# Kernel tuning notes

Hardware: AMD Instinct MI355X
Metric: run time of the kernel (lower is better)

Reference implementation:

```python
import jax, jax.numpy as jnp
import numpy as np

B, T, HOP = 4, 200, 120
N = T * HOP
M1, A1 = 40, 5            # mcep_order+1, apdc_order+1
HID, COND = 256, 192
SR = 24000.0
ALPHA = 0.466             # frequency-warping for 24 kHz
PD = 4                    # Pade order
PADE = jnp.asarray([1.0, 0.4999273, 0.1067005, 0.00956526, 0.0003041358], jnp.float32)
SIGN = jnp.asarray([1.0, -1.0, 1.0, -1.0], jnp.float32)  # + for odd Pade tap index
F0_MEAN, F0_STD = 5.0, 0.25
MCEP_MEAN, MCEP_STD = 0.0, 1.0
APDC_MEAN, APDC_STD = 0.0, 1.0
NOISE_RATIO, SP_RATE, F0_RATE = 0.5, 1.0, 1.0


def mc2b(mc, a):
    """SPTK mc2b: mel-cepstrum -> MLSA filter coefficients (scan over order)."""
    mc_rev = jnp.moveaxis(mc, -1, 0)[::-1]  # [M1, B, T]
    def step(carry, c):
        b = c - a * carry
        return b, b
    _, bs = jax.lax.scan(step, jnp.zeros_like(mc_rev[0]), mc_rev)
    return jnp.moveaxis(bs[::-1], 0, -1)


def _mlsafir(x, b, d):
    # SPTK mlsafir, vectorized over the PD Pade taps.
    # x: [PD], b: [M1], d: [PD, M1+1]
    aa = 1.0 - ALPHA * ALPHA
    d1 = aa * x + ALPHA * d[:, 1]
    def step(prev, di):  # d_new[i] = d[i] + a*(d[i+1] - d_new[i-1]) : order recurrence
        d_i, d_ip1 = di
        new = d_i + ALPHA * (d_ip1 - prev)
        return new, new
    xs = (d[:, 2:M1].T, d[:, 3:M1 + 1].T)  # [M1-2, PD]
    _, dupd = jax.lax.scan(step, d1, xs)    # [M1-2, PD]
    y = jnp.einsum('mp,m->p', dupd, b[2:])
    # delay-line shift: new d = [x, d1, d1, dupd[2..M]]
    new_d = jnp.concatenate([x[:, None], d1[:, None], d1[:, None], dupd.T], axis=1)
    return y, new_d


def _mlsa_step(state, inp):
    d1a, d1b, d2, pt2 = state
    x, b = inp
    x = x * jnp.exp(b[0])           # gain
    # ---- stage 1 (uses b[1] only), SPTK mlsadf1 ----
    aa = 1.0 - ALPHA * ALPHA
    na = aa * d1b[:PD] + ALPHA * d1a[1:]
    npt = na * b[1]
    v1 = npt * PADE[1:]
    x1 = x + jnp.sum(v1 * SIGN)
    y1 = jnp.sum(v1) + x1
    d1a = jnp.concatenate([d1a[:1], na])
    d1b = jnp.concatenate([x1[None], npt])
    # ---- stage 2 (orders >= 2), SPTK mlsadf2 ----
    fy, d2 = _mlsafir(pt2[:PD], b, d2)
    v2 = fy * PADE[1:]
    x2 = y1 + jnp.sum(v2 * SIGN)
    y2 = jnp.sum(v2) + x2
    pt2 = jnp.concatenate([x2[None], fy])
    return (d1a, d1b, d2, pt2), y2


def mlsa_filter(exc, b_up):
    # exc: [N], b_up: [N, M1] -> filtered waveform [N]
    init = (jnp.zeros(PD + 1, jnp.float32), jnp.zeros(PD + 1, jnp.float32),
            jnp.zeros((PD, M1 + 1), jnp.float32), jnp.zeros(PD + 1, jnp.float32))
    _, y = jax.lax.scan(_mlsa_step, init, (exc, b_up))
    return y


def _forward(mceps, apdcs, frame_f0s, noise,
             Wm, bm, Wa, ba, Wf, bf, Wpa, bpa, Wpp, bpp,
             Wrp, brp, Wra, bra, Wap):
    # linear feature embed + sum
    hs = mceps @ Wm + bm + apdcs @ Wa + ba + frame_f0s @ Wf + bf   # [B,T,HID]
    ca = hs @ Wpa + bpa                                             # prenet_a cond [B,T,COND]
    cp = hs @ Wpp + bpp                                             # prenet_p cond
    # denorm (+ exp for log-f0)
    f0 = jnp.exp(frame_f0s[..., 0] * F0_STD + F0_MEAN) * F0_RATE    # [B,T]
    sp = mceps * MCEP_STD + MCEP_MEAN
    ap = apdcs * APDC_STD + APDC_MEAN
    # per-path mel-cepstra with prenet residuals
    mc_p = sp * SP_RATE + 0.1 * jnp.tanh(cp @ Wrp + brp)
    mc_a = sp * SP_RATE + 0.1 * jnp.tanh(ca @ Wra + bra) + ap @ Wap
    b_p = mc2b(mc_p, ALPHA)
    b_a = mc2b(mc_a, ALPHA)
    # excitation at sample rate
    f0_up = jnp.repeat(f0, HOP, axis=1)                             # [B,N]
    phase = jnp.cumsum(f0_up / SR, axis=1)
    w = jnp.floor(phase)
    wprev = jnp.concatenate([jnp.zeros_like(w[:, :1]), w[:, :-1]], axis=1)
    amp = jnp.sqrt(SR / jnp.maximum(f0_up, 1.0))
    pulse = jnp.where(w > wprev, amp, 0.0)
    exc_p = pulse * (1.0 - NOISE_RATIO)
    exc_a = noise * NOISE_RATIO
    # run both (periodic/aperiodic) MLSA synthesis filters in one batched scan
    excs = jnp.concatenate([exc_p, exc_a], axis=0)                  # [2B,N]
    bs = jnp.repeat(jnp.concatenate([b_p, b_a], axis=0), HOP, axis=1)  # [2B,N,M1]
    wavs = jax.vmap(mlsa_filter)(excs, bs)                          # [2B,N]
    return wavs[:B] + wavs[B:]


_forward_jit = jax.jit(_forward)


def setup_inputs() -> dict:
    key = jax.random.key(0)
    ks = jax.random.split(key, 20)
    decay = 0.3 / (1.0 + jnp.arange(M1, dtype=jnp.float32))  # realistic cepstral decay (filter stability)
    return {
        'mceps': jax.random.normal(ks[0], (B, T, M1), jnp.float32) * decay,
        'apdcs': jax.random.normal(ks[1], (B, T, A1), jnp.float32) * 0.3,
        'frame_f0s': jax.random.normal(ks[2], (B, T, 1), jnp.float32),
        'noise': jax.random.normal(ks[3], (B, N), jnp.float32),
        'Wm': jax.random.normal(ks[4], (M1, HID), jnp.float32) / np.sqrt(M1),
        'bm': jnp.zeros((HID,), jnp.float32),
        'Wa': jax.random.normal(ks[5], (A1, HID), jnp.float32) / np.sqrt(A1),
        'ba': jnp.zeros((HID,), jnp.float32),
        'Wf': jax.random.normal(ks[6], (1, HID), jnp.float32),
        'bf': jnp.zeros((HID,), jnp.float32),
        'Wpa': jax.random.normal(ks[7], (HID, COND), jnp.float32) / np.sqrt(HID),
        'bpa': jnp.zeros((COND,), jnp.float32),
        'Wpp': jax.random.normal(ks[8], (HID, COND), jnp.float32) / np.sqrt(HID),
        'bpp': jnp.zeros((COND,), jnp.float32),
        'Wrp': jax.random.normal(ks[9], (COND, M1), jnp.float32) / np.sqrt(COND),
        'brp': jnp.zeros((M1,), jnp.float32),
        'Wra': jax.random.normal(ks[10], (COND, M1), jnp.float32) / np.sqrt(COND),
        'bra': jnp.zeros((M1,), jnp.float32),
        'Wap': jax.random.normal(ks[11], (A1, M1), jnp.float32) * 0.05,
    }


def reference(mceps, apdcs, frame_f0s, noise,
              Wm, bm, Wa, ba, Wf, bf, Wpa, bpa, Wpp, bpp,
              Wrp, brp, Wra, bra, Wap):
    return _forward_jit(mceps, apdcs, frame_f0s, noise,
                        Wm, bm, Wa, ba, Wf, bf, Wpa, bpa, Wpp, bpp,
                        Wrp, brp, Wra, bra, Wap)
```

## Files before the change

### kernel.cpp

```cpp
#include <hip/hip_runtime.h>
#include <math.h>

#define ALPHA 0.466f
#define T_FRAMES 200
#define HOPW 120
#define NSAMP 24000
#define M1 40
#define HID 256
#define CONDW 192

#define NCHUNK 200
#define WARMF 4
#define SERF (WARMF + 1)
#define WARMK0 96

#define F8 8
#define EMB_BLOCKS (4 * T_FRAMES / F8)
#define BPF ((NSAMP + 255) / 256)

#if defined(__has_builtin)
#  if __has_builtin(__builtin_amdgcn_permlane32_swap)
#    define HAVE_PLSWAP 1
#  endif
#endif
#ifndef HAVE_PLSWAP
#  define HAVE_PLSWAP 0
#endif

__global__ __launch_bounds__(256) void prep_kernel(
    const float* __restrict__ mceps, const float* __restrict__ apdcs,
    const float* __restrict__ f0s, const float* __restrict__ noise,
    const float* __restrict__ Wm, const float* __restrict__ bm,
    const float* __restrict__ Wa, const float* __restrict__ ba,
    const float* __restrict__ Wf, const float* __restrict__ bf,
    const float* __restrict__ Wpa, const float* __restrict__ bpa,
    const float* __restrict__ Wpp, const float* __restrict__ bpp,
    const float* __restrict__ Wrp, const float* __restrict__ brp,
    const float* __restrict__ Wra, const float* __restrict__ bra,
    const float* __restrict__ Wap,
    float* __restrict__ bcoef, float* __restrict__ exc)
{
    const int tid = threadIdx.x;

    if (blockIdx.x >= EMB_BLOCKS) {
        const int xb = blockIdx.x - EMB_BLOCKS;
        const int ff = xb / BPF;
        const int n = (xb % BPF) * 256 + tid;

        if (ff >= 4) {
            if (n < NSAMP) exc[ff * NSAMP + n] = 0.5f * noise[(ff - 4) * NSAMP + n];
            return;
        }

        __shared__ double s_base[T_FRAMES];
        __shared__ double s_step[T_FRAMES];
        __shared__ float  s_amp[T_FRAMES];

        if (tid < 64) {
            const int L = tid;
            double st[4], loc[4];
            float am[4];
            double s = 0.0;
            #pragma unroll
            for (int j = 0; j < 4; ++j) {
                int ft = L * 4 + j;
                if (ft < T_FRAMES) {
                    double fv = exp((double)f0s[ff * T_FRAMES + ft] * 0.25 + 5.0);
                    st[j] = fv / 24000.0;
                    am[j] = (float)(0.5 * sqrt(24000.0 / fmax(fv, 1.0)));
                } else { st[j] = 0.0; am[j] = 0.f; }
                loc[j] = s;
                s += st[j];
            }
            double tot = s;
            #pragma unroll
            for (int off = 1; off < 64; off <<= 1) {
                double v = __shfl_up(s, off, 64);
                if (L >= off) s += v;
            }
            double excl = s - tot;
            #pragma unroll
            for (int j = 0; j < 4; ++j) {
                int ft = L * 4 + j;
                if (ft < T_FRAMES) {
                    s_base[ft] = 120.0 * (excl + loc[j]);
                    s_step[ft] = st[j];
                    s_amp[ft]  = am[j];
                }
            }
        }
        __syncthreads();

        if (n < NSAMP) {
            int ft = n / HOPW, k = n - ft * HOPW;
            double st = s_step[ft], bs = s_base[ft];
            double ph  = bs + (double)(k + 1) * st;
            double php = bs + (double)k * st;
            exc[ff * NSAMP + n] = (floor(ph) > floor(php)) ? s_amp[ft] : 0.0f;
        }
        return;
    }

    __shared__ float s_mc[F8][M1];
    __shared__ float s_ap[F8][5];
    __shared__ float s_f0[F8];
    __shared__ float s_h[F8][HID];
    __shared__ float s_ca[F8][CONDW];
    __shared__ float s_cp[F8][CONDW];
    __shared__ float s_mcp[F8][M1];
    __shared__ float s_mca[F8][M1];

    const int R0 = blockIdx.x * F8;

    for (int j = tid; j < F8 * M1; j += 256) s_mc[j / M1][j % M1] = mceps[R0 * M1 + j];
    if (tid < F8 * 5) s_ap[tid / 5][tid % 5] = apdcs[R0 * 5 + tid];
    if (tid < F8)     s_f0[tid] = f0s[R0 + tid];
    __syncthreads();

    {
        float acc[F8];
        const float bias = bm[tid] + ba[tid] + bf[tid];
        #pragma unroll
        for (int r = 0; r < F8; ++r) acc[r] = bias;
        for (int k = 0; k < M1; ++k) {
            float w = Wm[k * HID + tid];
            #pragma unroll
            for (int r = 0; r < F8; ++r) acc[r] = fmaf(s_mc[r][k], w, acc[r]);
        }
        #pragma unroll
        for (int k = 0; k < 5; ++k) {
            float w = Wa[k * HID + tid];
            #pragma unroll
            for (int r = 0; r < F8; ++r) acc[r] = fmaf(s_ap[r][k], w, acc[r]);
        }
        float wf = Wf[tid];
        #pragma unroll
        for (int r = 0; r < F8; ++r) s_h[r][tid] = fmaf(s_f0[r], wf, acc[r]);
    }
    __syncthreads();

    if (tid < CONDW) {
        float aA[F8], aP[F8];
        #pragma unroll
        for (int r = 0; r < F8; ++r) { aA[r] = bpa[tid]; aP[r] = bpp[tid]; }
        for (int k = 0; k < HID; k += 4) {
            float4 h4[F8];
            #pragma unroll
            for (int r = 0; r < F8; ++r) h4[r] = *(const float4*)&s_h[r][k];
            #pragma unroll
            for (int kk = 0; kk < 4; ++kk) {
                float wa = Wpa[(k + kk) * CONDW + tid];
                float wp = Wpp[(k + kk) * CONDW + tid];
                #pragma unroll
                for (int r = 0; r < F8; ++r) {
                    float hv = (&h4[r].x)[kk];
                    aA[r] = fmaf(hv, wa, aA[r]);
                    aP[r] = fmaf(hv, wp, aP[r]);
                }
            }
        }
        #pragma unroll
        for (int r = 0; r < F8; ++r) { s_ca[r][tid] = aA[r]; s_cp[r][tid] = aP[r]; }
    }
    __syncthreads();

    if (tid < M1) {
        const int u = tid;
        float acc[F8];
        #pragma unroll
        for (int r = 0; r < F8; ++r) acc[r] = brp[u];
        for (int k = 0; k < CONDW; k += 4) {
            float4 c4[F8];
            #pragma unroll
            for (int r = 0; r < F8; ++r) c4[r] = *(const float4*)&s_cp[r][k];
            #pragma unroll
            for (int kk = 0; kk < 4; ++kk) {
                float w = Wrp[(k + kk) * M1 + u];
                #pragma unroll
                for (int r = 0; r < F8; ++r) acc[r] = fmaf((&c4[r].x)[kk], w, acc[r]);
            }
        }
        #pragma unroll
        for (int r = 0; r < F8; ++r)
            s_mcp[r][u] = s_mc[r][u] + 0.1f * tanhf(acc[r]);
    } else if (tid >= 64 && tid < 64 + M1) {
        const int u = tid - 64;
        float acc[F8];
        #pragma unroll
        for (int r = 0; r < F8; ++r) acc[r] = bra[u];
        for (int k = 0; k < CONDW; k += 4) {
            float4 c4[F8];
            #pragma unroll
            for (int r = 0; r < F8; ++r) c4[r] = *(const float4*)&s_ca[r][k];
            #pragma unroll
            for (int kk = 0; kk < 4; ++kk) {
                float w = Wra[(k + kk) * M1 + u];
                #pragma unroll
                for (int r = 0; r < F8; ++r) acc[r] = fmaf((&c4[r].x)[kk], w, acc[r]);
            }
        }
        #pragma unroll
        for (int r = 0; r < F8; ++r) {
            float aw = 0.f;
            #pragma unroll
            for (int j = 0; j < 5; ++j) aw = fmaf(s_ap[r][j], Wap[j * M1 + u], aw);
            s_mca[r][u] = s_mc[r][u] + 0.1f * tanhf(acc[r]) + aw;
        }
    }
    __syncthreads();

    if (tid < 16) {
        const int r = tid >> 1, path = tid & 1;
        const int R = R0 + r;
        const int batch = R / T_FRAMES, t = R - batch * T_FRAMES;
        const float* src = path ? s_mca[r] : s_mcp[r];
        float* dst = bcoef + ((path * 4 + batch) * T_FRAMES + t) * M1;
        float prev = src[M1 - 1];
        dst[M1 - 1] = prev;
        for (int m = M1 - 2; m >= 0; --m) {
            prev = src[m] - ALPHA * prev;
            dst[m] = prev;
        }
    }
}

template <int CTRL>
__device__ __forceinline__ float rshr(float x) {
    return __int_as_float(
        __builtin_amdgcn_mov_dpp(__float_as_int(x), CTRL, 0xF, 0xF, true));
}
__device__ __forceinline__ float rlane(float x, int l) {
    return __int_as_float(__builtin_amdgcn_readlane(__float_as_int(x), l));
}
__device__ __forceinline__ float vpin(float x) {
    asm("" : "+v"(x));
    return x;
}

template <bool OUT, int KSTART>
__device__ __forceinline__ void run_frame(
    const float* __restrict__ sx, float AB,
    float BP1, float BP2, float BP3, float BP4,
    float B0, float B1, float B2, float B3, float B4,
    float K, float IPw, bool pos0, bool row0, bool parodd,
    float& E0, float& E1, float& E2, float& E3, float& E4,
    float& dlp, float& xin,
    float& m1, float& m2, float& m3, float& m4, float& w0,
    float* __restrict__ yb)
{
    const float A   = ALPHA;
    const float AA  = 1.0f - A * A;
    const float A2  = A * A;
    const float mA3 = -(A * A2);
    const float A4  = A2 * A2;
    const float R   = -(A4 * A);
    const float R2  = R * R;

    const float Rv   = vpin(R);
    const float R2v  = vpin(R2);
    const float IPwv = vpin(IPw);

    #pragma unroll 1
    for (int k8 = KSTART; k8 < HOPW; k8 += 8) {
        const float4 g0 = *(const float4*)&sx[k8];
        const float4 g1 = *(const float4*)&sx[k8 + 4];
        const float xs[8] = {g0.x, g0.y, g0.z, g0.w, g1.x, g1.y, g1.z, g1.w};
        #pragma unroll
        for (int j = 0; j < 8; ++j) {
            float x = xs[j];

            float na0 = fmaf(A, m1, AA * w0);
            float na1 = fmaf(A, m2, AB * m1);
            float na2 = fmaf(A, m3, AB * m2);
            float na3 = fmaf(A, m4, AB * m3);
            float p = fmaf(na2, BP3, na0 * BP1);
            float q = fmaf(na3, BP4, na1 * BP2);
            float x1 = x + (p - q);
            float y1 = fmaf(2.0f, p, x);
            m1 = na0; m2 = na1; m3 = na2; m4 = na3; w0 = x1;

            float pE4 = rshr<0x112>(E4);
            float c0 = fmaf(A, E0, pos0 ? dlp : pE4);
            float c1 = fmaf(A, E1, E0);
            float c2 = fmaf(A, E2, E1);
            float c3 = fmaf(A, E3, E2);
            float c4 = fmaf(A, E4, E3);
            float u0 = c0;
            float u1 = fmaf(-A, u0, c1);
            float u2 = fmaf(-A, u1, c2);
            float u3 = fmaf(-A, u2, c3);
            float u4 = fmaf(-A, u3, c4);
            float X = u4;
            X = fmaf(rshr<0x112>(X), Rv,  X);
            X = fmaf(rshr<0x114>(X), R2v, X);
            float dl = fmaf(AA, xin, A * dlp);
            float Xt = fmaf(K, dl, X);
            float Si = rshr<0x112>(Xt);
            Si = pos0 ? dl : Si;
            float t0 = fmaf(-A,  Si, u0);
            float t1 = fmaf(A2,  Si, u1);
            float t2 = fmaf(mA3, Si, u2);
            float t3 = fmaf(A4,  Si, u3);

            float fp = t0 * B0;
            fp = fmaf(t1, B1, fp);
            fp = fmaf(t2, B2, fp);
            fp = fmaf(t3, B3, fp);
            fp = fmaf(Xt, B4, fp);
            float S = fp;
            S += rshr<0x112>(S);
            S += rshr<0x114>(S);
            S += rshr<0x118>(S);

            float Sx  = rshr<0x111>(S);
            float T1m = rshr<0x142>(S)  * IPwv;
            float T0m = rshr<0x142>(Sx) * IPwv;
            float xprev = parodd ? T1m : T0m;

#if HAVE_PLSWAP
            typedef unsigned u32x2 __attribute__((ext_vector_type(2)));
            u32x2 rr = __builtin_amdgcn_permlane32_swap(
                __float_as_uint(S), __float_as_uint(S), false, false);
            float S2 = __uint_as_float(rr.x) + __uint_as_float(rr.y);
            float aE = rlane(S2, 14), bE = rlane(S2, 30);
            float aO = rlane(S2, 15), bO = rlane(S2, 31);
            float tot = parodd ? (aO + bO) : (aE + bE);
            float x2 = y1 + tot;
            if (OUT) {
                float dif = parodd ? (aO - bO) : (aE - bE);
                yb[k8 + j] = x2 + dif;
            }
#else
            float s0p = rlane(S, 14), s1p = rlane(S, 30);
            float s2p = rlane(S, 46), s3p = rlane(S, 62);
            float s0a = rlane(S, 15), s1a = rlane(S, 31);
            float s2a = rlane(S, 47), s3a = rlane(S, 63);
            float eP = s0p + s2p, oP = s1p + s3p;
            float eA = s0a + s2a, oA = s1a + s3a;
            float ce = parodd ? eA : eP;
            float co = parodd ? oA : oP;
            float x2 = y1 + (ce + co);
            if (OUT) yb[k8 + j] = x2 + (ce - co);
#endif

            xin = row0 ? x2 : xprev;
            E0 = t0; E1 = t1; E2 = t2; E3 = t3; E4 = Xt;
            dlp = dl;
        }
    }
}

__global__ __launch_bounds__(64) void mlsa_kernel(
    const float* __restrict__ bcoef, const float* __restrict__ exc,
    float* __restrict__ out)
{
    __shared__ __align__(16) float sexc[2][HOPW + 4];
    __shared__ __align__(16) float ybuf[2][HOPW + 4];

    const int tid = threadIdx.x;
    const int par = tid & 1;
    const int pos = (tid >> 1) & 7;
    const int row = tid >> 4;
    const int chunk = blockIdx.x >> 2;
    const int b = blockIdx.x & 3;
    const int f = par * 4 + b;
    const bool pos0 = (pos == 0), row0 = (row == 0), parodd = (par != 0);

    const float P1 = 0.4999273f, P2 = 0.1067005f, P3 = 0.00956526f, P4 = 0.0003041358f;
    const float wrow = (row == 0) ? P1 : (row == 1) ? -P2 : (row == 2) ? P3 : -P4;
    const float IPw  = (row == 1) ? (1.f / P1) : (row == 2) ? (-1.f / P2)
                     : (row == 3) ? (1.f / P3) : 0.f;

    const float A = ALPHA;
    const float R = -(A * A * A * A * A);
    float K = R;
    for (int j = 0; j < pos; ++j) K *= R;

    float E0 = 0.f, E1 = 0.f, E2 = 0.f, E3 = 0.f, E4 = 0.f;
    float dlp = 0.f, xin = 0.f;
    float m1 = 0.f, m2 = 0.f, m3 = 0.f, m4 = 0.f, w0 = 0.f;

    const float* sxp = sexc[par];
    float* ybp = ybuf[par];
    const int ja = 5 * pos + 2;
    const int lh = tid >> 1;

    #pragma unroll 1
    for (int i = 0; i < SERF; ++i) {
        const int ftA = chunk - WARMF + i;
        const int ftc = (ftA < 0) ? 0 : ftA;
        const float* bp = bcoef + (f * T_FRAMES + ftc) * M1;
        const float b1 = bp[1];
        const float G  = expf(bp[0]);
        const float AAc = 1.0f - A * A;
        const float AB = AAc * b1;
        const float BP1 = b1 * P1, BP2 = b1 * P2, BP3 = b1 * P3, BP4 = b1 * P4;

        const float* ex = exc + f * NSAMP + ftc * HOPW;
        #pragma unroll
        for (int m = 0; m < 4; ++m) {
            int kk = lh + 32 * m;
            if (kk < HOPW) sexc[par][kk] = (ftA >= 0) ? ex[kk] * G : 0.f;
        }

        const float B0c = bp[ja]     * wrow;
        const float B1c = bp[ja + 1] * wrow;
        const float B2c = bp[ja + 2] * wrow;
        const float B3c = (pos < 7) ? bp[ja + 3] * wrow : 0.f;
        const float B4c = (pos < 7) ? bp[ja + 4] * wrow : 0.f;

        if (i == 0) {
            run_frame<false, WARMK0>(sxp, AB, BP1, BP2, BP3, BP4,
                            B0c, B1c, B2c, B3c, B4c, K, IPw, pos0, row0, parodd,
                            E0, E1, E2, E3, E4, dlp, xin, m1, m2, m3, m4, w0, ybp);
        } else if (i < SERF - 1) {
            run_frame<false, 0>(sxp, AB, BP1, BP2, BP3, BP4,
                            B0c, B1c, B2c, B3c, B4c, K, IPw, pos0, row0, parodd,
                            E0, E1, E2, E3, E4, dlp, xin, m1, m2, m3, m4, w0, ybp);
        } else {
            run_frame<true, 0>(sxp, AB, BP1, BP2, BP3, BP4,
                            B0c, B1c, B2c, B3c, B4c, K, IPw, pos0, row0, parodd,
                            E0, E1, E2, E3, E4, dlp, xin, m1, m2, m3, m4, w0, ybp);
            float* op = out + b * NSAMP + chunk * HOPW;
            op[tid] = ybuf[0][tid] + ybuf[1][tid];
            if (tid < HOPW - 64) op[tid + 64] = ybuf[0][tid + 64] + ybuf[1][tid + 64];
        }
    }
}

extern "C" void kernel_launch(void* const* d_in, const int* in_sizes, int n_in,
                              void* d_out, int out_size, void* d_ws, size_t ws_size,
                              hipStream_t stream) {
    const float* mceps = (const float*)d_in[0];
    const float* apdcs = (const float*)d_in[1];
    const float* f0s   = (const float*)d_in[2];
    const float* noise = (const float*)d_in[3];
    const float* Wm  = (const float*)d_in[4];
    const float* bm  = (const float*)d_in[5];
    const float* Wa  = (const float*)d_in[6];
    const float* ba  = (const float*)d_in[7];
    const float* Wf  = (const float*)d_in[8];
    const float* bf  = (const float*)d_in[9];
    const float* Wpa = (const float*)d_in[10];
    const float* bpa = (const float*)d_in[11];
    const float* Wpp = (const float*)d_in[12];
    const float* bpp = (const float*)d_in[13];
    const float* Wrp = (const float*)d_in[14];
    const float* brp = (const float*)d_in[15];
    const float* Wra = (const float*)d_in[16];
    const float* bra = (const float*)d_in[17];
    const float* Wap = (const float*)d_in[18];
    float* out = (float*)d_out;

    char* ws = (char*)d_ws;
    float* bcoef = (float*)(ws + 0);
    float* exc   = (float*)(ws + 256000);

    prep_kernel<<<dim3(EMB_BLOCKS + 8 * BPF), dim3(256), 0, stream>>>(
        mceps, apdcs, f0s, noise, Wm, bm, Wa, ba, Wf, bf,
        Wpa, bpa, Wpp, bpp, Wrp, brp, Wra, bra, Wap, bcoef, exc);

    mlsa_kernel<<<dim3(NCHUNK * 4), dim3(64), 0, stream>>>(bcoef, exc, out);
}
```

Measured before the change: 196.3 us.

## Take dl-dependent term off the critical path by linearizing the FIR dot-product reduction

Rewrites the per-sample stage-2 filter so that the cross-lane dot-product reduction no longer waits on the delayed input dl. The dot product and its DPP reduction are computed from X and its lane-shifted value. The dl contribution is then added afterward through a per-frame precomputed coefficient CKp, itself reduced across lanes once per frame. This shortens the serial dependency chain per sample, at the cost of a few extra per-frame setup instructions and some floating-point reassociation.

After: 198.8 us. About the same (+1.3%).

```diff
diff --git a/kernel.cpp b/kernel.cpp
--- a/kernel.cpp
+++ b/kernel.cpp
@@ -242,7 +242,8 @@
     const float* __restrict__ sx, float AB,
     float BP1, float BP2, float BP3, float BP4,
     float B0, float B1, float B2, float B3, float B4,
-    float K, float IPw, bool pos0, bool row0, bool parodd,
+    float GBv, float CKp, float K, float KS, float IPw,
+    bool pos0, bool row0, bool parodd,
     float& E0, float& E1, float& E2, float& E3, float& E4,
     float& dlp, float& xin,
     float& m1, float& m2, float& m3, float& m4, float& w0,
@@ -293,24 +294,27 @@
             float X = u4;
             X = fmaf(rshr<0x112>(X), Rv,  X);
             X = fmaf(rshr<0x114>(X), R2v, X);
+            float XS = rshr<0x112>(X);
+            float fpX = u0 * B0;
+            fpX = fmaf(u1, B1, fpX);
+            fpX = fmaf(u2, B2, fpX);
+            fpX = fmaf(u3, B3, fpX);
+            fpX = fmaf(X,  B4, fpX);
+            fpX = fmaf(XS, GBv, fpX);
+            float SX = fpX;
+            SX += rshr<0x112>(SX);
+            SX += rshr<0x114>(SX);
+            SX += rshr<0x118>(SX);
+
             float dl = fmaf(AA, xin, A * dlp);
+            float S  = fmaf(dl, CKp, SX);
+
+            float Si = fmaf(KS, dl, XS);
             float Xt = fmaf(K, dl, X);
-            float Si = rshr<0x112>(Xt);
-            Si = pos0 ? dl : Si;
             float t0 = fmaf(-A,  Si, u0);
             float t1 = fmaf(A2,  Si, u1);
             float t2 = fmaf(mA3, Si, u2);
             float t3 = fmaf(A4,  Si, u3);
-
-            float fp = t0 * B0;
-            fp = fmaf(t1, B1, fp);
-            fp = fmaf(t2, B2, fp);
-            fp = fmaf(t3, B3, fp);
-            fp = fmaf(Xt, B4, fp);
-            float S = fp;
-            S += rshr<0x112>(S);
-            S += rshr<0x114>(S);
-            S += rshr<0x118>(S);
 
             float Sx  = rshr<0x111>(S);
             float T1m = rshr<0x142>(S)  * IPwv;
@@ -372,9 +376,13 @@
                      : (row == 3) ? (1.f / P3) : 0.f;
 
     const float A = ALPHA;
-    const float R = -(A * A * A * A * A);
-    float K = R;
-    for (int j = 0; j < pos; ++j) K *= R;
+    const float A2c = A * A;
+    const float mA3c = -(A * A2c);
+    const float A4c = A2c * A2c;
+    const float R = -(A4c * A);
+    float KS = 1.f;
+    for (int j = 0; j < pos; ++j) KS *= R;
+    const float K = KS * R;
 
     float E0 = 0.f, E1 = 0.f, E2 = 0.f, E3 = 0.f, E4 = 0.f;
     float dlp = 0.f, xin = 0.f;
@@ -409,17 +417,27 @@
         const float B3c = (pos < 7) ? bp[ja + 3] * wrow : 0.f;
         const float B4c = (pos < 7) ? bp[ja + 4] * wrow : 0.f;
 
+        const float GBc = fmaf(A4c, B3c, fmaf(mA3c, B2c, fmaf(A2c, B1c, -A * B0c)));
+        const float fpK = fmaf(K, B4c, KS * GBc);
+        float CKp = fpK;
+        CKp += rshr<0x112>(CKp);
+        CKp += rshr<0x114>(CKp);
+        CKp += rshr<0x118>(CKp);
+
         if (i == 0) {
             run_frame<false, WARMK0>(sxp, AB, BP1, BP2, BP3, BP4,
-                            B0c, B1c, B2c, B3c, B4c, K, IPw, pos0, row0, parodd,
+                            B0c, B1c, B2c, B3c, B4c, GBc, CKp, K, KS, IPw,
+                            pos0, row0, parodd,
                             E0, E1, E2, E3, E4, dlp, xin, m1, m2, m3, m4, w0, ybp);
         } else if (i < SERF - 1) {
             run_frame<false, 0>(sxp, AB, BP1, BP2, BP3, BP4,
-                            B0c, B1c, B2c, B3c, B4c, K, IPw, pos0, row0, parodd,
+                            B0c, B1c, B2c, B3c, B4c, GBc, CKp, K, KS, IPw,
+                            pos0, row0, parodd,
                             E0, E1, E2, E3, E4, dlp, xin, m1, m2, m3, m4, w0, ybp);
         } else {
             run_frame<true, 0>(sxp, AB, BP1, BP2, BP3, BP4,
-                            B0c, B1c, B2c, B3c, B4c, K, IPw, pos0, row0, parodd,
+                            B0c, B1c, B2c, B3c, B4c, GBc, CKp, K, KS, IPw,
+                            pos0, row0, parodd,
                             E0, E1, E2, E3, E4, dlp, xin, m1, m2, m3, m4, w0, ybp);
             float* op = out + b * NSAMP + chunk * HOPW;
             op[tid] = ybuf[0][tid] + ybuf[1][tid];
```
